# Kernel optimization log

Measured on AMD Instinct MI355X. Metric: run time of the kernel, lower is better.

Reference implementation:

```python
import jax, jax.numpy as jnp
import numpy as np

B, T, S, D, H, DK, DV = 4, 2048, 2048, 1024, 16, 64, 64


def setup_inputs() -> dict:
    key = jax.random.key(0)
    ks = jax.random.split(key, 12)
    sq = 1.0 / np.sqrt(D)
    return {
        "query": jax.random.normal(ks[0], (B, T, D), jnp.float32),
        "value": jax.random.normal(ks[1], (B, S, D), jnp.float32),
        "mask": jnp.ones((B, T, S), dtype=bool),
        "Wq": jax.random.normal(ks[2], (D, H, DK), jnp.float32) * sq,
        "bq": jnp.zeros((H, DK), jnp.float32),
        "Wk": jax.random.normal(ks[3], (D, H, DK), jnp.float32) * sq,
        "bk": jnp.zeros((H, DK), jnp.float32),
        "Wv": jax.random.normal(ks[4], (D, H, DV), jnp.float32) * sq,
        "bv": jnp.zeros((H, DV), jnp.float32),
        "Wo": jax.random.normal(ks[5], (H, DV, D), jnp.float32) * (1.0 / np.sqrt(H * DV)),
        "bo": jnp.zeros((D,), jnp.float32),
    }


def reference(query, value, mask, Wq, bq, Wk, bk, Wv, bv, Wo, bo):
    # key input defaults to value when only [query, value] is given
    q = jnp.einsum("btd,dhk->bthk", query, Wq) + bq  # [B,T,H,DK]
    k = jnp.einsum("bsd,dhk->bshk", value, Wk) + bk  # [B,S,H,DK]
    v = jnp.einsum("bsd,dhv->bshv", value, Wv) + bv  # [B,S,H,DV]
    # dot_product_equation 'aecd,abcd->acbe': scores[b,h,t,s]
    scores = jnp.einsum("bshk,bthk->bhts", k, q) * (1.0 / np.sqrt(DK))
    # MaskedSoftmax: mask [B,T,S] expanded at axis 1 -> [B,1,T,S]
    adder = (1.0 - mask[:, None, :, :].astype(scores.dtype)) * -10000.0
    probs = jax.nn.softmax(scores + adder, axis=-1)
    # combine_equation 'acbe,aecd->abcd'
    attn = jnp.einsum("bhts,bshv->bthv", probs, v)  # [B,T,H,DV]
    out = jnp.einsum("bthv,hvd->btd", attn, Wo) + bo  # [B,T,D]
    return out
```

## Files before the change

### kernel.cpp

```cpp
#include <hip/hip_runtime.h>

typedef __bf16 bf16x8 __attribute__((ext_vector_type(8)));
typedef __bf16 bf16x4 __attribute__((ext_vector_type(4)));
typedef float  f32x4  __attribute__((ext_vector_type(4)));
typedef int    i32x4  __attribute__((ext_vector_type(4)));

typedef __attribute__((address_space(1))) unsigned int as1_u32;
typedef __attribute__((address_space(3))) unsigned int as3_u32;

#define DEVI __device__ __forceinline__

DEVI unsigned short f2bf(float f) {
    union { float f; unsigned u; } v; v.f = f;
    unsigned r = (v.u + 0x7fffu + ((v.u >> 16) & 1u)) >> 16;
    return (unsigned short)r;
}

DEVI void gload16(const void* g, void* l) {
    __builtin_amdgcn_global_load_lds((const as1_u32*)g, (as3_u32*)l, 16, 0, 0);
}

#define C_EXP 0.18033688011112042f
#define MASK_ADD (-14426.950408889634f)

__global__ __launch_bounds__(256) void cvt_kernel(const float* __restrict__ in,
                                                  unsigned short* __restrict__ out,
                                                  int n8) {
    const int stride = gridDim.x * 256;
    for (int idx = blockIdx.x * 256 + threadIdx.x; idx < n8; idx += stride) {
        const f32x4 a = *(const f32x4*)(in + (size_t)idx * 8);
        const f32x4 b = *(const f32x4*)(in + (size_t)idx * 8 + 4);
        union { bf16x4 v[2]; i32x4 q; } u;
        u.v[0] = __builtin_convertvector(a, bf16x4);
        u.v[1] = __builtin_convertvector(b, bf16x4);
        *(i32x4*)(out + (size_t)idx * 8) = u.q;
    }
}

__global__ __launch_bounds__(256) void wtrans_kernel(const float* __restrict__ W0,
                                                     const float* __restrict__ W1,
                                                     const float* __restrict__ W2,
                                                     const float* __restrict__ W3,
                                                     unsigned short* __restrict__ T0,
                                                     unsigned short* __restrict__ T1,
                                                     unsigned short* __restrict__ T2,
                                                     unsigned short* __restrict__ T3) {
    __shared__ float tile[64][65];
    const float* W;
    unsigned short* WT;
    float scale = 1.0f;
    switch (blockIdx.z) {
        case 0:  W = W0; WT = T0; scale = C_EXP; break;
        case 1:  W = W1; WT = T1; break;
        case 2:  W = W2; WT = T2; break;
        default: W = W3; WT = T3; break;
    }
    const int k0 = blockIdx.x * 64, n0 = blockIdx.y * 64;
    const int i = threadIdx.x;
    const int c4 = (i & 15) * 4, rbase = i >> 4;
    for (int rr = 0; rr < 4; ++rr) {
        const int kl = rbase + rr * 16;
        const float4 v = *(const float4*)(W + (size_t)(k0 + kl) * 1024 + n0 + c4);
        tile[kl][c4 + 0] = v.x; tile[kl][c4 + 1] = v.y;
        tile[kl][c4 + 2] = v.z; tile[kl][c4 + 3] = v.w;
    }
    __syncthreads();
    for (int rr = 0; rr < 4; ++rr) {
        const int nl = rbase + rr * 16;
        ushort4 o;
        o.x = f2bf(tile[c4 + 0][nl] * scale); o.y = f2bf(tile[c4 + 1][nl] * scale);
        o.z = f2bf(tile[c4 + 2][nl] * scale); o.w = f2bf(tile[c4 + 3][nl] * scale);
        *(ushort4*)(WT + (size_t)(n0 + nl) * 1024 + k0 + c4) = o;
    }
}

__global__ __launch_bounds__(256) void maskflag_kernel(const int* __restrict__ mask,
                                                       unsigned* __restrict__ flagsW) {
    const int bid = blockIdx.x;
    const int b = bid >> 9, rem = bid & 511;
    const int tb = rem >> 5, si = rem & 31;
    const int i = threadIdx.x;
    const int t = tb * 128 + (i >> 1);
    const int s = si * 64 + (i & 1) * 32;
    const uint4* p = (const uint4*)(mask + ((size_t)(b * 2048 + t)) * 2048 + s);
    int ok = 1;
    #pragma unroll
    for (int u = 0; u < 8; ++u) {
        const uint4 a = p[u];
        ok &= (a.x != 0) & (a.y != 0) & (a.z != 0) & (a.w != 0);
    }
    int all = __syncthreads_and(ok);
    if (i == 0 && !all) atomicOr(&flagsW[b * 16 + tb], 1u << si);
}

template <int MODE, int NB>
__global__ __launch_bounds__(256) void mm_kernel(const unsigned short* __restrict__ A,
                                                 const unsigned short* __restrict__ BT,
                                                 const float* __restrict__ biasK,
                                                 const float* __restrict__ biasV,
                                                 float bscale,
                                                 void* __restrict__ OvK,
                                                 void* __restrict__ OvV) {
    __shared__ __align__(16) unsigned short Ab[2][128 * 64];
    __shared__ __align__(16) unsigned short Bb[2][128 * 64];
    const int bid = blockIdx.x;
    const int xcd = bid & 7, jj = bid >> 3;
    const int n0 = (jj % NB) * 128;
    const int m0 = ((jj / NB) * 8 + xcd) * 128;
    const int i = threadIdx.x, w = i >> 6, l = i & 63;
    const int wm = w >> 1, wn = w & 1;
    const int c = l & 15, g = l >> 4;
    const int srow = l >> 3, sslot = l & 7;

    f32x4 acc[4][4] = {};

    const unsigned short* As[4];
    const unsigned short* Bs[4];
    unsigned lofs[4];
    #pragma unroll
    for (int u = 0; u < 4; ++u) {
        const int rl = w * 32 + u * 8 + srow;
        const int ch = sslot ^ ((rl ^ (rl >> 2)) & 7);
        As[u] = A  + (size_t)(m0 + rl) * 1024 + ch * 8;
        Bs[u] = BT + (size_t)(n0 + rl) * 1024 + ch * 8;
        lofs[u] = (unsigned)((w * 32 + u * 8) * 64);
    }

    #pragma unroll
    for (int u = 0; u < 4; ++u) {
        gload16(As[u], &Ab[0][lofs[u]]);
        gload16(Bs[u], &Bb[0][lofs[u]]);
    }
    __syncthreads();

    int rsA[4], rsB[4];
    #pragma unroll
    for (int f = 0; f < 4; ++f) {
        const int ra = wm * 64 + f * 16 + c;
        const int rb = wn * 64 + f * 16 + c;
        rsA[f] = (ra ^ (ra >> 2)) & 7;
        rsB[f] = (rb ^ (rb >> 2)) & 7;
    }

    #pragma unroll 2
    for (int it = 0; it < 16; ++it) {
        const int buf = it & 1;
        if (it < 15) {
            #pragma unroll
            for (int u = 0; u < 4; ++u) {
                gload16(As[u] + (it + 1) * 64, &Ab[buf ^ 1][lofs[u]]);
                gload16(Bs[u] + (it + 1) * 64, &Bb[buf ^ 1][lofs[u]]);
            }
        }
        bf16x8 af[4][2], bfr[4][2];
        #pragma unroll
        for (int f = 0; f < 4; ++f)
            #pragma unroll
            for (int kk = 0; kk < 2; ++kk) {
                af[f][kk]  = *(const bf16x8*)&Ab[buf][(wm * 64 + f * 16 + c) * 64 + (((kk * 4 + g) ^ rsA[f]) * 8)];
                bfr[f][kk] = *(const bf16x8*)&Bb[buf][(wn * 64 + f * 16 + c) * 64 + (((kk * 4 + g) ^ rsB[f]) * 8)];
            }
        __builtin_amdgcn_s_setprio(1);
        #pragma unroll
        for (int kk = 0; kk < 2; ++kk)
            #pragma unroll
            for (int mf = 0; mf < 4; ++mf)
                #pragma unroll
                for (int nf = 0; nf < 4; ++nf)
                    acc[mf][nf] = __builtin_amdgcn_mfma_f32_16x16x32_bf16(af[mf][kk], bfr[nf][kk], acc[mf][nf], 0, 0, 0);
        __builtin_amdgcn_s_setprio(0);
        __syncthreads();
    }

    #pragma unroll
    for (int nf = 0; nf < 4; ++nf) {
        const int n = n0 + wn * 64 + nf * 16 + c;
        if (MODE == 0 || (MODE == 3 && n0 < 1024)) {
            const float bv = biasK[n] * bscale;
            const int h = n >> 6, cc = n & 63;
            unsigned short* O = (unsigned short*)OvK;
            #pragma unroll
            for (int mf = 0; mf < 4; ++mf) {
                const int mbase = m0 + wm * 64 + mf * 16 + g * 4;
                const int b = mbase >> 11, t = mbase & 2047;
                #pragma unroll
                for (int r = 0; r < 4; ++r)
                    O[(((size_t)(b * 16 + h)) * 2048 + t + r) * 64 + cc] = f2bf(acc[mf][nf][r] + bv);
            }
        } else if (MODE == 3) {
            const int nn = n - 1024;
            const float bv = biasV[nn];
            const int h = nn >> 6, cc = nn & 63;
            unsigned short* O = (unsigned short*)OvV;
            #pragma unroll
            for (int mf = 0; mf < 4; ++mf) {
                const int mbase = m0 + wm * 64 + mf * 16 + g * 4;
                const int b = mbase >> 11, t = mbase & 2047;
                f32x4 v;
                #pragma unroll
                for (int r = 0; r < 4; ++r) v[r] = acc[mf][nf][r] + bv;
                bf16x4 pv = __builtin_convertvector(v, bf16x4);
                *(bf16x4*)(O + (((size_t)(b * 16 + h)) * 64 + cc) * 2048 + t) = pv;
            }
        } else {
            const float bv = biasK[n] * bscale;
            float* O = (float*)OvK;
            #pragma unroll
            for (int mf = 0; mf < 4; ++mf) {
                const int mbase = m0 + wm * 64 + mf * 16 + g * 4;
                #pragma unroll
                for (int r = 0; r < 4; ++r)
                    O[(size_t)(mbase + r) * 1024 + n] = acc[mf][nf][r] + bv;
            }
        }
    }
}

__global__ __launch_bounds__(256, 4) void attn_kernel(const unsigned short* __restrict__ Qp,
                                                      const unsigned short* __restrict__ Kp,
                                                      const unsigned short* __restrict__ VTp,
                                                      const int* __restrict__ mask,
                                                      const unsigned* __restrict__ flagsW,
                                                      unsigned short* __restrict__ attnb) {
    __shared__ __align__(16) unsigned short Kt[2][64 * 64];
    __shared__ __align__(16) unsigned short Vt[2][64 * 64];

    const int bid = blockIdx.x;
    const int xcd = bid & 7, jj = bid >> 3;
    const int bh = xcd * 8 + (jj >> 4);
    const int tb = jj & 15;
    const int b = bh >> 4, h = bh & 15;
    const int i = threadIdx.x, w = i >> 6, l = i & 63;
    const int c = l & 15, g = l >> 4;

    const unsigned short* Qb  = Qp  + (size_t)bh * 2048 * 64;
    const unsigned short* Kb  = Kp  + (size_t)bh * 2048 * 64;
    const unsigned short* VTb = VTp + (size_t)bh * 64 * 2048;

    const int twave = tb * 128 + w * 32;
    const int tA = twave + c, tB = twave + 16 + c;

    const unsigned notall = __builtin_amdgcn_readfirstlane(flagsW[b * 16 + tb]);

    bf16x8 qfA[2], qfB[2];
    #pragma unroll
    for (int kq = 0; kq < 2; ++kq) {
        qfA[kq] = *(const bf16x8*)(Qb + (size_t)tA * 64 + kq * 32 + g * 8);
        qfB[kq] = *(const bf16x8*)(Qb + (size_t)tB * 64 + kq * 32 + g * 8);
    }

    f32x4 oA[4] = {}, oB[4] = {};
    f32x4 daccA = {}, daccB = {};
    const f32x4 zf = {};

    bf16x8 ones8;
    #pragma unroll
    for (int j = 0; j < 8; ++j) ones8[j] = (__bf16)1.0f;

    int rrow[4], rswz[4];
    #pragma unroll
    for (int sm = 0; sm < 4; ++sm) {
        rrow[sm] = (sm >> 1) * 32 + (c >> 2) * 8 + (sm & 1) * 4 + (c & 3);
        rswz[sm] = (rrow[sm] ^ (rrow[sm] >> 2)) & 7;
    }
    int vswz[4];
    #pragma unroll
    for (int vm = 0; vm < 4; ++vm) {
        const int rv = vm * 16 + c;
        vswz[vm] = (rv ^ (rv >> 2)) & 7;
    }

    const int srow = l >> 3, sslot = l & 7;

    const unsigned short* kstage[2];
    const unsigned short* vstage[2];
    #pragma unroll
    for (int u = 0; u < 2; ++u) {
        const int row = w * 16 + u * 8 + srow;
        const int ch = sslot ^ ((row ^ (row >> 2)) & 7);
        gload16(Kb + (size_t)row * 64 + ch * 8, &Kt[0][(w * 16 + u * 8) * 64]);
        gload16(VTb + (size_t)row * 2048 + ch * 8, &Vt[0][(w * 16 + u * 8) * 64]);
        kstage[u] = Kb + (size_t)(64 + row) * 64 + ch * 8;
        vstage[u] = VTb + (size_t)row * 2048 + 64 + ch * 8;
    }
    __syncthreads();

    #pragma unroll 2
    for (int it = 0; it < 32; ++it) {
        const int buf = it & 1;
        const int s0 = it * 64;

        if (it < 31) {
            #pragma unroll
            for (int u = 0; u < 2; ++u) {
                gload16(kstage[u], &Kt[buf ^ 1][(w * 16 + u * 8) * 64]);
                gload16(vstage[u], &Vt[buf ^ 1][(w * 16 + u * 8) * 64]);
                kstage[u] += 64 * 64;
                vstage[u] += 64;
            }
        }

        f32x4 scA[4], scB[4];
        __builtin_amdgcn_s_setprio(1);
        #pragma unroll
        for (int sm = 0; sm < 4; ++sm) {
            #pragma unroll
            for (int kq = 0; kq < 2; ++kq) {
                const bf16x8 kf = *(const bf16x8*)&Kt[buf][rrow[sm] * 64 + (((kq * 4 + g) ^ rswz[sm]) * 8)];
                if (kq == 0) {
                    scA[sm] = __builtin_amdgcn_mfma_f32_16x16x32_bf16(kf, qfA[0], zf, 0, 0, 0);
                    scB[sm] = __builtin_amdgcn_mfma_f32_16x16x32_bf16(kf, qfB[0], zf, 0, 0, 0);
                } else {
                    scA[sm] = __builtin_amdgcn_mfma_f32_16x16x32_bf16(kf, qfA[1], scA[sm], 0, 0, 0);
                    scB[sm] = __builtin_amdgcn_mfma_f32_16x16x32_bf16(kf, qfB[1], scB[sm], 0, 0, 0);
                }
            }
        }
        __builtin_amdgcn_s_setprio(0);

        if (notall & (1u << it)) {
            #pragma unroll
            for (int sm = 0; sm < 4; ++sm)
                #pragma unroll
                for (int r = 0; r < 4; ++r) {
                    const int s = s0 + (sm >> 1) * 32 + g * 8 + (sm & 1) * 4 + r;
                    if (mask[(size_t)(b * 2048 + tA) * 2048 + s] == 0) scA[sm][r] += MASK_ADD;
                    if (mask[(size_t)(b * 2048 + tB) * 2048 + s] == 0) scB[sm][r] += MASK_ADD;
                }
        }

        bf16x8 paA[2], paB[2];
        #pragma unroll
        for (int kv = 0; kv < 2; ++kv) {
            f32x4 a0, a1, b0, b1;
            #pragma unroll
            for (int r = 0; r < 4; ++r) {
                a0[r] = __builtin_amdgcn_exp2f(scA[kv * 2][r]);
                a1[r] = __builtin_amdgcn_exp2f(scA[kv * 2 + 1][r]);
                b0[r] = __builtin_amdgcn_exp2f(scB[kv * 2][r]);
                b1[r] = __builtin_amdgcn_exp2f(scB[kv * 2 + 1][r]);
            }
            union { struct { bf16x4 lo, hi; } hh; bf16x8 v; } ua, ub;
            ua.hh.lo = __builtin_convertvector(a0, bf16x4);
            ua.hh.hi = __builtin_convertvector(a1, bf16x4);
            ub.hh.lo = __builtin_convertvector(b0, bf16x4);
            ub.hh.hi = __builtin_convertvector(b1, bf16x4);
            paA[kv] = ua.v;
            paB[kv] = ub.v;
        }

        __builtin_amdgcn_s_setprio(1);
        #pragma unroll
        for (int kv = 0; kv < 2; ++kv) {
            daccA = __builtin_amdgcn_mfma_f32_16x16x32_bf16(ones8, paA[kv], daccA, 0, 0, 0);
            daccB = __builtin_amdgcn_mfma_f32_16x16x32_bf16(ones8, paB[kv], daccB, 0, 0, 0);
            #pragma unroll
            for (int vm = 0; vm < 4; ++vm) {
                const bf16x8 vf = *(const bf16x8*)&Vt[buf][(vm * 16 + c) * 64 + (((kv * 4 + g) ^ vswz[vm]) * 8)];
                oA[vm] = __builtin_amdgcn_mfma_f32_16x16x32_bf16(vf, paA[kv], oA[vm], 0, 0, 0);
                oB[vm] = __builtin_amdgcn_mfma_f32_16x16x32_bf16(vf, paB[kv], oB[vm], 0, 0, 0);
            }
        }
        __builtin_amdgcn_s_setprio(0);

        __syncthreads();
    }

    const float invA = 1.0f / daccA[0];
    const float invB = 1.0f / daccB[0];

    #pragma unroll
    for (int vm = 0; vm < 4; ++vm) {
        f32x4 vA, vB;
        #pragma unroll
        for (int r = 0; r < 4; ++r) { vA[r] = oA[vm][r] * invA; vB[r] = oB[vm][r] * invB; }
        bf16x4 pA = __builtin_convertvector(vA, bf16x4);
        bf16x4 pB = __builtin_convertvector(vB, bf16x4);
        *(bf16x4*)(attnb + (size_t)(b * 2048 + tA) * 1024 + h * 64 + vm * 16 + g * 4) = pA;
        *(bf16x4*)(attnb + (size_t)(b * 2048 + tB) * 1024 + h * 64 + vm * 16 + g * 4) = pB;
    }
}

extern "C" void kernel_launch(void* const* d_in, const int* in_sizes, int n_in,
                              void* d_out, int out_size, void* d_ws, size_t ws_size,
                              hipStream_t stream) {
    const float* query = (const float*)d_in[0];
    const float* value = (const float*)d_in[1];
    const int*   mask  = (const int*)d_in[2];
    const float* Wq = (const float*)d_in[3];
    const float* bq = (const float*)d_in[4];
    const float* Wk = (const float*)d_in[5];
    const float* bk = (const float*)d_in[6];
    const float* Wv = (const float*)d_in[7];
    const float* bv = (const float*)d_in[8];
    const float* Wo = (const float*)d_in[9];
    const float* bo = (const float*)d_in[10];

    char* ws = (char*)d_ws;
    unsigned short* WqT   = (unsigned short*)(ws + ((size_t)0  << 20));
    unsigned short* WkT   = (unsigned short*)(ws + ((size_t)2  << 20));
    unsigned short* WvT   = (unsigned short*)(ws + ((size_t)4  << 20));
    unsigned short* WoT   = (unsigned short*)(ws + ((size_t)6  << 20));
    unsigned*       flagsW= (unsigned*)      (ws + ((size_t)8  << 20));
    unsigned short* CONV  = (unsigned short*)(ws + ((size_t)9  << 20));
    unsigned short* Qp    = (unsigned short*)(ws + ((size_t)25 << 20));
    unsigned short* Kp    = (unsigned short*)(ws + ((size_t)41 << 20));
    unsigned short* VTp   = (unsigned short*)(ws + ((size_t)57 << 20));

    const int n8 = 8192 * 1024 / 8;

    hipMemsetAsync(flagsW, 0, 64 * sizeof(unsigned), stream);

    cvt_kernel<<<2048, 256, 0, stream>>>(value, CONV, n8);
    wtrans_kernel<<<dim3(16, 16, 4), 256, 0, stream>>>(Wq, Wk, Wv, Wo, WqT, WkT, WvT, WoT);
    maskflag_kernel<<<2048, 256, 0, stream>>>(mask, flagsW);
    mm_kernel<3, 16><<<1024, 256, 0, stream>>>(CONV, WkT, bk, bv, 1.0f, Kp, VTp);

    cvt_kernel<<<2048, 256, 0, stream>>>(query, CONV, n8);
    mm_kernel<0, 8><<<512, 256, 0, stream>>>(CONV, WqT, bq, bq, C_EXP, Qp, nullptr);

    attn_kernel<<<1024, 256, 0, stream>>>(Qp, Kp, VTp, mask, flagsW, CONV);

    mm_kernel<2, 8><<<512, 256, 0, stream>>>(CONV, WoT, bo, bo, 1.0f, d_out, nullptr);
}
```

Baseline: 204.5 us.

## Halve GEMM K-tile to 32 and pipeline loads with explicit vmcnt waits

The projection GEMM kernel now stages 128x32 bf16 tiles instead of 128x64, halving shared memory per block. It adds a launch-bounds minimum of 5 blocks per SM to raise occupancy. The main loop now issues next-tile global-to-LDS loads before waiting with a partial vmcnt, which lets the current tile's MFMAs overlap outstanding loads, and the final tile is peeled out of the loop. The trade-off is twice as many barriers per K and less MFMA work per synchronisation, plus tighter register limits.

```diff
diff --git a/kernel.cpp b/kernel.cpp
--- a/kernel.cpp
+++ b/kernel.cpp
@@ -94,15 +94,15 @@
 }
 
 template <int MODE, int NB>
-__global__ __launch_bounds__(256) void mm_kernel(const unsigned short* __restrict__ A,
-                                                 const unsigned short* __restrict__ BT,
-                                                 const float* __restrict__ biasK,
-                                                 const float* __restrict__ biasV,
-                                                 float bscale,
-                                                 void* __restrict__ OvK,
-                                                 void* __restrict__ OvV) {
-    __shared__ __align__(16) unsigned short Ab[2][128 * 64];
-    __shared__ __align__(16) unsigned short Bb[2][128 * 64];
+__global__ __launch_bounds__(256, 5) void mm_kernel(const unsigned short* __restrict__ A,
+                                                    const unsigned short* __restrict__ BT,
+                                                    const float* __restrict__ biasK,
+                                                    const float* __restrict__ biasV,
+                                                    float bscale,
+                                                    void* __restrict__ OvK,
+                                                    void* __restrict__ OvV) {
+    __shared__ __align__(16) unsigned short Ab[2][128 * 32];
+    __shared__ __align__(16) unsigned short Bb[2][128 * 32];
     const int bid = blockIdx.x;
     const int xcd = bid & 7, jj = bid >> 3;
     const int n0 = (jj % NB) * 128;
@@ -110,66 +110,77 @@
     const int i = threadIdx.x, w = i >> 6, l = i & 63;
     const int wm = w >> 1, wn = w & 1;
     const int c = l & 15, g = l >> 4;
-    const int srow = l >> 3, sslot = l & 7;
 
     f32x4 acc[4][4] = {};
 
-    const unsigned short* As[4];
-    const unsigned short* Bs[4];
-    unsigned lofs[4];
-    #pragma unroll
-    for (int u = 0; u < 4; ++u) {
-        const int rl = w * 32 + u * 8 + srow;
-        const int ch = sslot ^ ((rl ^ (rl >> 2)) & 7);
+    const int srow4 = l >> 2, sslot4 = l & 3;
+    const unsigned short* As[2];
+    const unsigned short* Bs[2];
+    unsigned lofs[2];
+    #pragma unroll
+    for (int u = 0; u < 2; ++u) {
+        const int rl = w * 32 + u * 16 + srow4;
+        const int ch = sslot4 ^ ((rl ^ (rl >> 2)) & 3);
         As[u] = A  + (size_t)(m0 + rl) * 1024 + ch * 8;
         Bs[u] = BT + (size_t)(n0 + rl) * 1024 + ch * 8;
-        lofs[u] = (unsigned)((w * 32 + u * 8) * 64);
-    }
-
-    #pragma unroll
-    for (int u = 0; u < 4; ++u) {
-        gload16(As[u], &Ab[0][lofs[u]]);
-        gload16(Bs[u], &Bb[0][lofs[u]]);
-    }
-    __syncthreads();
+        lofs[u] = (unsigned)((w * 32 + u * 16) * 32);
+    }
 
     int rsA[4], rsB[4];
     #pragma unroll
     for (int f = 0; f < 4; ++f) {
         const int ra = wm * 64 + f * 16 + c;
         const int rb = wn * 64 + f * 16 + c;
-        rsA[f] = (ra ^ (ra >> 2)) & 7;
-        rsB[f] = (rb ^ (rb >> 2)) & 7;
+        rsA[f] = (ra ^ (ra >> 2)) & 3;
+        rsB[f] = (rb ^ (rb >> 2)) & 3;
+    }
+
+    #pragma unroll
+    for (int u = 0; u < 2; ++u) {
+        gload16(As[u], &Ab[0][lofs[u]]);
+        gload16(Bs[u], &Bb[0][lofs[u]]);
     }
 
     #pragma unroll 2
-    for (int it = 0; it < 16; ++it) {
-        const int buf = it & 1;
-        if (it < 15) {
-            #pragma unroll
-            for (int u = 0; u < 4; ++u) {
-                gload16(As[u] + (it + 1) * 64, &Ab[buf ^ 1][lofs[u]]);
-                gload16(Bs[u] + (it + 1) * 64, &Bb[buf ^ 1][lofs[u]]);
-            }
-        }
-        bf16x8 af[4][2], bfr[4][2];
-        #pragma unroll
-        for (int f = 0; f < 4; ++f)
-            #pragma unroll
-            for (int kk = 0; kk < 2; ++kk) {
-                af[f][kk]  = *(const bf16x8*)&Ab[buf][(wm * 64 + f * 16 + c) * 64 + (((kk * 4 + g) ^ rsA[f]) * 8)];
-                bfr[f][kk] = *(const bf16x8*)&Bb[buf][(wn * 64 + f * 16 + c) * 64 + (((kk * 4 + g) ^ rsB[f]) * 8)];
-            }
+    for (int it = 0; it < 31; ++it) {
+        const int bufc = it & 1, bufn = bufc ^ 1;
+        #pragma unroll
+        for (int u = 0; u < 2; ++u) {
+            gload16(As[u] + (it + 1) * 32, &Ab[bufn][lofs[u]]);
+            gload16(Bs[u] + (it + 1) * 32, &Bb[bufn][lofs[u]]);
+        }
+        asm volatile("s_waitcnt vmcnt(4)" ::: "memory");
+        __builtin_amdgcn_s_barrier();
+        bf16x8 af[4], bfr[4];
+        #pragma unroll
+        for (int f = 0; f < 4; ++f) {
+            af[f]  = *(const bf16x8*)&Ab[bufc][(wm * 64 + f * 16 + c) * 32 + ((g ^ rsA[f]) * 8)];
+            bfr[f] = *(const bf16x8*)&Bb[bufc][(wn * 64 + f * 16 + c) * 32 + ((g ^ rsB[f]) * 8)];
+        }
         __builtin_amdgcn_s_setprio(1);
         #pragma unroll
-        for (int kk = 0; kk < 2; ++kk)
-            #pragma unroll
-            for (int mf = 0; mf < 4; ++mf)
-                #pragma unroll
-                for (int nf = 0; nf < 4; ++nf)
-                    acc[mf][nf] = __builtin_amdgcn_mfma_f32_16x16x32_bf16(af[mf][kk], bfr[nf][kk], acc[mf][nf], 0, 0, 0);
+        for (int mf = 0; mf < 4; ++mf)
+            #pragma unroll
+            for (int nf = 0; nf < 4; ++nf)
+                acc[mf][nf] = __builtin_amdgcn_mfma_f32_16x16x32_bf16(af[mf], bfr[nf], acc[mf][nf], 0, 0, 0);
         __builtin_amdgcn_s_setprio(0);
-        __syncthreads();
+        asm volatile("s_waitcnt lgkmcnt(0)" ::: "memory");
+        __builtin_amdgcn_s_barrier();
+    }
+    {
+        asm volatile("s_waitcnt vmcnt(0)" ::: "memory");
+        __builtin_amdgcn_s_barrier();
+        bf16x8 af[4], bfr[4];
+        #pragma unroll
+        for (int f = 0; f < 4; ++f) {
+            af[f]  = *(const bf16x8*)&Ab[1][(wm * 64 + f * 16 + c) * 32 + ((g ^ rsA[f]) * 8)];
+            bfr[f] = *(const bf16x8*)&Bb[1][(wn * 64 + f * 16 + c) * 32 + ((g ^ rsB[f]) * 8)];
+        }
+        #pragma unroll
+        for (int mf = 0; mf < 4; ++mf)
+            #pragma unroll
+            for (int nf = 0; nf < 4; ++nf)
+                acc[mf][nf] = __builtin_amdgcn_mfma_f32_16x16x32_bf16(af[mf], bfr[nf], acc[mf][nf], 0, 0, 0);
     }
 
     #pragma unroll
```

Measured after the change: 419.9 us. 2.05x slower.

## Fuse fp32-to-bf16 input conversion into projection GEMM A-tile loads

Applied to the files above, without the earlier changes.

Drops the two standalone conversion kernels for value and query. The K/V and Q projection GEMMs now read fp32 activations straight into registers, convert them to bf16 and write them to LDS, with the next tile prefetched into registers during the MFMA loop. This removes two kernel launches and the bf16 intermediate write and read. In exchange the GEMM reads twice as many bytes per A element, and it replaces async global-to-LDS loads with register staging and explicit LDS stores, which adds register pressure.

```diff
diff --git a/kernel.cpp b/kernel.cpp
--- a/kernel.cpp
+++ b/kernel.cpp
@@ -22,20 +22,6 @@
 
 #define C_EXP 0.18033688011112042f
 #define MASK_ADD (-14426.950408889634f)
-
-__global__ __launch_bounds__(256) void cvt_kernel(const float* __restrict__ in,
-                                                  unsigned short* __restrict__ out,
-                                                  int n8) {
-    const int stride = gridDim.x * 256;
-    for (int idx = blockIdx.x * 256 + threadIdx.x; idx < n8; idx += stride) {
-        const f32x4 a = *(const f32x4*)(in + (size_t)idx * 8);
-        const f32x4 b = *(const f32x4*)(in + (size_t)idx * 8 + 4);
-        union { bf16x4 v[2]; i32x4 q; } u;
-        u.v[0] = __builtin_convertvector(a, bf16x4);
-        u.v[1] = __builtin_convertvector(b, bf16x4);
-        *(i32x4*)(out + (size_t)idx * 8) = u.q;
-    }
-}
 
 __global__ __launch_bounds__(256) void wtrans_kernel(const float* __restrict__ W0,
                                                      const float* __restrict__ W1,
@@ -93,8 +79,8 @@
     if (i == 0 && !all) atomicOr(&flagsW[b * 16 + tb], 1u << si);
 }
 
-template <int MODE, int NB>
-__global__ __launch_bounds__(256) void mm_kernel(const unsigned short* __restrict__ A,
+template <int MODE, int NB, int AF32>
+__global__ __launch_bounds__(256) void mm_kernel(const void* __restrict__ Av,
                                                  const unsigned short* __restrict__ BT,
                                                  const float* __restrict__ biasK,
                                                  const float* __restrict__ biasV,
@@ -114,24 +100,22 @@
 
     f32x4 acc[4][4] = {};
 
-    const unsigned short* As[4];
+    int arow[4];
+    int achunk[4];
     const unsigned short* Bs[4];
     unsigned lofs[4];
     #pragma unroll
     for (int u = 0; u < 4; ++u) {
         const int rl = w * 32 + u * 8 + srow;
         const int ch = sslot ^ ((rl ^ (rl >> 2)) & 7);
-        As[u] = A  + (size_t)(m0 + rl) * 1024 + ch * 8;
+        arow[u] = rl;
+        achunk[u] = ch;
         Bs[u] = BT + (size_t)(n0 + rl) * 1024 + ch * 8;
-        lofs[u] = (unsigned)((w * 32 + u * 8) * 64);
-    }
-
-    #pragma unroll
-    for (int u = 0; u < 4; ++u) {
-        gload16(As[u], &Ab[0][lofs[u]]);
-        gload16(Bs[u], &Bb[0][lofs[u]]);
-    }
-    __syncthreads();
+        lofs[u] = (unsigned)(rl * 64);
+    }
+
+    const float* Af = (const float*)Av;
+    const unsigned short* Ab16 = (const unsigned short*)Av;
 
     int rsA[4], rsB[4];
     #pragma unroll
@@ -142,16 +126,51 @@
         rsB[f] = (rb ^ (rb >> 2)) & 7;
     }
 
+    #pragma unroll
+    for (int u = 0; u < 4; ++u)
+        gload16(Bs[u], &Bb[0][(w * 32 + u * 8) * 64]);
+    if (AF32) {
+        #pragma unroll
+        for (int u = 0; u < 4; ++u) {
+            const float* src = Af + (size_t)(m0 + arow[u]) * 1024 + achunk[u] * 8;
+            const f32x4 lo = *(const f32x4*)(src);
+            const f32x4 hi = *(const f32x4*)(src + 4);
+            union { struct { bf16x4 lo, hi; } h; i32x4 q; } uu;
+            uu.h.lo = __builtin_convertvector(lo, bf16x4);
+            uu.h.hi = __builtin_convertvector(hi, bf16x4);
+            *(i32x4*)&Ab[0][lofs[u] + sslot * 8] = uu.q;
+        }
+    } else {
+        #pragma unroll
+        for (int u = 0; u < 4; ++u)
+            gload16(Ab16 + (size_t)(m0 + arow[u]) * 1024 + achunk[u] * 8,
+                    &Ab[0][(w * 32 + u * 8) * 64]);
+    }
+    __syncthreads();
+
     #pragma unroll 2
     for (int it = 0; it < 16; ++it) {
         const int buf = it & 1;
+        f32x4 areg[4][2];
         if (it < 15) {
             #pragma unroll
-            for (int u = 0; u < 4; ++u) {
-                gload16(As[u] + (it + 1) * 64, &Ab[buf ^ 1][lofs[u]]);
-                gload16(Bs[u] + (it + 1) * 64, &Bb[buf ^ 1][lofs[u]]);
-            }
-        }
+            for (int u = 0; u < 4; ++u)
+                gload16(Bs[u] + (it + 1) * 64, &Bb[buf ^ 1][(w * 32 + u * 8) * 64]);
+            if (AF32) {
+                #pragma unroll
+                for (int u = 0; u < 4; ++u) {
+                    const float* src = Af + (size_t)(m0 + arow[u]) * 1024 + (it + 1) * 64 + achunk[u] * 8;
+                    areg[u][0] = *(const f32x4*)(src);
+                    areg[u][1] = *(const f32x4*)(src + 4);
+                }
+            } else {
+                #pragma unroll
+                for (int u = 0; u < 4; ++u)
+                    gload16(Ab16 + (size_t)(m0 + arow[u]) * 1024 + (it + 1) * 64 + achunk[u] * 8,
+                            &Ab[buf ^ 1][(w * 32 + u * 8) * 64]);
+            }
+        }
+
         bf16x8 af[4][2], bfr[4][2];
         #pragma unroll
         for (int f = 0; f < 4; ++f)
@@ -169,6 +188,16 @@
                 for (int nf = 0; nf < 4; ++nf)
                     acc[mf][nf] = __builtin_amdgcn_mfma_f32_16x16x32_bf16(af[mf][kk], bfr[nf][kk], acc[mf][nf], 0, 0, 0);
         __builtin_amdgcn_s_setprio(0);
+
+        if (AF32 && it < 15) {
+            #pragma unroll
+            for (int u = 0; u < 4; ++u) {
+                union { struct { bf16x4 lo, hi; } h; i32x4 q; } uu;
+                uu.h.lo = __builtin_convertvector(areg[u][0], bf16x4);
+                uu.h.hi = __builtin_convertvector(areg[u][1], bf16x4);
+                *(i32x4*)&Ab[buf ^ 1][lofs[u] + sslot * 8] = uu.q;
+            }
+        }
         __syncthreads();
     }
 
@@ -402,24 +431,20 @@
     unsigned short* WvT   = (unsigned short*)(ws + ((size_t)4  << 20));
     unsigned short* WoT   = (unsigned short*)(ws + ((size_t)6  << 20));
     unsigned*       flagsW= (unsigned*)      (ws + ((size_t)8  << 20));
-    unsigned short* CONV  = (unsigned short*)(ws + ((size_t)9  << 20));
+    unsigned short* attnb = (unsigned short*)(ws + ((size_t)9  << 20));
     unsigned short* Qp    = (unsigned short*)(ws + ((size_t)25 << 20));
     unsigned short* Kp    = (unsigned short*)(ws + ((size_t)41 << 20));
     unsigned short* VTp   = (unsigned short*)(ws + ((size_t)57 << 20));
 
-    const int n8 = 8192 * 1024 / 8;
-
     hipMemsetAsync(flagsW, 0, 64 * sizeof(unsigned), stream);
 
-    cvt_kernel<<<2048, 256, 0, stream>>>(value, CONV, n8);
     wtrans_kernel<<<dim3(16, 16, 4), 256, 0, stream>>>(Wq, Wk, Wv, Wo, WqT, WkT, WvT, WoT);
     maskflag_kernel<<<2048, 256, 0, stream>>>(mask, flagsW);
-    mm_kernel<3, 16><<<1024, 256, 0, stream>>>(CONV, WkT, bk, bv, 1.0f, Kp, VTp);
-
-    cvt_kernel<<<2048, 256, 0, stream>>>(query, CONV, n8);
-    mm_kernel<0, 8><<<512, 256, 0, stream>>>(CONV, WqT, bq, bq, C_EXP, Qp, nullptr);
-
-    attn_kernel<<<1024, 256, 0, stream>>>(Qp, Kp, VTp, mask, flagsW, CONV);
-
-    mm_kernel<2, 8><<<512, 256, 0, stream>>>(CONV, WoT, bo, bo, 1.0f, d_out, nullptr);
-}
+
+    mm_kernel<3, 16, 1><<<1024, 256, 0, stream>>>(value, WkT, bk, bv, 1.0f, Kp, VTp);
+    mm_kernel<0, 8, 1><<<512, 256, 0, stream>>>(query, WqT, bq, bq, C_EXP, Qp, nullptr);
+
+    attn_kernel<<<1024, 256, 0, stream>>>(Qp, Kp, VTp, mask, flagsW, attnb);
+
+    mm_kernel<2, 8, 0><<<512, 256, 0, stream>>>(attnb, WoT, bo, bo, 1.0f, d_out, nullptr);
+}
```

Result: no change. 207.0 us (+1.2%).
